# Performance work log

Hardware: AMD Instinct MI355X
Metric: run time of the kernel (lower is better)

The kernel has to match this reference:

```python
import jax, jax.numpy as jnp
import numpy as np

FACTORS = (32, 32, 32)  # prod = 32768 feature dim
BATCH = 2048


def setup_inputs() -> dict:
    key = jax.random.key(0)
    k0, k1, k2, k3 = jax.random.split(key, 4)
    N = int(np.prod(FACTORS))
    x = jax.random.normal(k0, (BATCH, N), dtype=jnp.float32)
    # scale weights ~1/sqrt(f) so outputs stay O(1) through 3 contractions
    s = 1.0 / np.sqrt(FACTORS[0])
    W1 = jax.random.normal(k1, (FACTORS[0], FACTORS[0]), dtype=jnp.float32) * s
    W2 = jax.random.normal(k2, (FACTORS[1], FACTORS[1]), dtype=jnp.float32) * s
    W3 = jax.random.normal(k3, (FACTORS[2], FACTORS[2]), dtype=jnp.float32) * s
    return {"x": x, "W1": W1, "W2": W2, "W3": W3}


def reference(x, W1, W2, W3):
    # Factorized (Kronecker) linear: y = x with each factor axis contracted
    # against its factor matrix (x.view(-1, f) @ W_f per factor, axes cycled).
    B = x.shape[0]
    f1, f2, f3 = FACTORS
    x = x.reshape(B, f1, f2, f3)
    x = jnp.einsum('bpqr,pi->biqr', x, W1)  # contract factor-1 axis
    x = jnp.einsum('biqr,qj->bijr', x, W2)  # contract factor-2 axis
    x = jnp.einsum('bijr,rk->bijk', x, W3)  # contract factor-3 axis
    return x.reshape(B, f1 * f2 * f3)
```

## Files before the change

### kernel.cpp

```cpp
#include <hip/hip_runtime.h>
#include <hip/hip_bf16.h>


typedef __attribute__((ext_vector_type(8))) short bf16x8;
typedef __attribute__((ext_vector_type(4))) float f32x4;

#define NROW 32768
#define NBLK 512

#define BAR() do {                                          \
    asm volatile("s_waitcnt lgkmcnt(0)" ::: "memory");      \
    __builtin_amdgcn_s_barrier();                           \
    __builtin_amdgcn_sched_barrier(0);                      \
} while (0)

__device__ __forceinline__ unsigned pk2(float a, float b) {
    union { __hip_bfloat162 h; unsigned u; } v;
    v.h = __float22bfloat162_rn(make_float2(a, b));
    return v.u;
}
__device__ __forceinline__ unsigned short b16(float a) {
    union { __hip_bfloat16 h; unsigned short u; } v;
    v.h = __float2bfloat16(a);
    return v.u;
}
__device__ __forceinline__ bf16x8 packfrag(float4 f0, float4 f1) {
    union { unsigned u[4]; bf16x8 b; } r;
    r.u[0] = pk2(f0.x, f0.y); r.u[1] = pk2(f0.z, f0.w);
    r.u[2] = pk2(f1.x, f1.y); r.u[3] = pk2(f1.z, f1.w);
    return r.b;
}

__device__ __forceinline__ int swz(int row, int col) {
    int s = ((row ^ (row >> 2) ^ (row >> 4)) & 3) << 3;
    return row * 32 + (col ^ s);
}

__device__ __forceinline__ bf16x8 ldsfrag(const unsigned short* buf, int row, int g) {
    int s = (row ^ (row >> 2) ^ (row >> 4)) & 3;
    union { uint4 u; bf16x8 b; } cv;
    cv.u = *(const uint4*)(buf + row * 32 + 8 * (g ^ s));
    return cv.b;
}

__global__ __launch_bounds__(1024, 8) void kron3_mfma(
    const float* __restrict__ x,  const float* __restrict__ W1,
    const float* __restrict__ W2, const float* __restrict__ W3,
    float* __restrict__ out, int iters)
{
    __shared__ unsigned short buf[NROW];
    __shared__ unsigned short wlds[3 * 1024];
    const int t = threadIdx.x;
    const int w = t >> 6, c = t & 15, g = (t >> 4) & 3;
    const f32x4 vzero = {0.f, 0.f, 0.f, 0.f};

    {
        const int n = t >> 5, k = t & 31;
        wlds[0 * 1024 + swz(n, k)] = b16(W1[k * 32 + n]);
        wlds[1 * 1024 + swz(n, k)] = b16(W2[k * 32 + n]);
        wlds[2 * 1024 + swz(n, k)] = b16(W3[k * 32 + n]);
    }
    BAR();

#pragma unroll 1
    for (int it = 0; it < iters; ++it) {
        int tv = t;
        asm volatile("" : "+v"(tv));
        const int cv = tv & 15, gv = (tv >> 4) & 3;
        const size_t row = (size_t)blockIdx.x + (size_t)NBLK * it;

        bf16x8 fa[4];
        {
            const float* xr = x + row * NROW;
#pragma unroll
            for (int mt = 0; mt < 4; ++mt) {
                const float* s = xr + (64 * w + 16 * mt + c) * 32 + 8 * g;
                float4 f0 = ((const float4*)s)[0];
                float4 f1 = ((const float4*)s)[1];
                fa[mt] = packfrag(f0, f1);
            }
        }

        {
            bf16x8 wA0 = ldsfrag(wlds + 2048, cv, gv);
            bf16x8 wA1 = ldsfrag(wlds + 2048, 16 + cv, gv);
#pragma unroll
            for (int nt = 0; nt < 2; ++nt) {
                const int kp = 16 * nt + c;
                const bf16x8 wA = nt ? wA1 : wA0;
#pragma unroll
                for (int mt = 0; mt < 4; ++mt) {
                    f32x4 a = __builtin_amdgcn_mfma_f32_16x16x32_bf16(fa[mt], wA, vzero, 0, 0, 0);
                    const int p  = 2 * w + (mt >> 1);
                    const int q0 = 16 * (mt & 1) + 4 * g;
                    *(uint2*)(buf + swz(p * 32 + kp, q0)) =
                        make_uint2(pk2(a[0], a[1]), pk2(a[2], a[3]));
                }
            }
        }

        bf16x8 fb[4];
#pragma unroll
        for (int mt = 0; mt < 4; ++mt)
            fb[mt] = ldsfrag(buf, 64 * w + 16 * mt + c, g);
        BAR();

        {
            bf16x8 wB0 = ldsfrag(wlds + 1024, cv, gv);
            bf16x8 wB1 = ldsfrag(wlds + 1024, 16 + cv, gv);
#pragma unroll
            for (int jt = 0; jt < 2; ++jt) {
                const bf16x8 wB = jt ? wB1 : wB0;
#pragma unroll
                for (int mt = 0; mt < 4; ++mt) {
                    f32x4 a = __builtin_amdgcn_mfma_f32_16x16x32_bf16(wB, fb[mt], vzero, 0, 0, 0);
                    const int k = 16 * (mt & 1) + c;
                    const int p = 2 * w + (mt >> 1);
#pragma unroll
                    for (int rg = 0; rg < 4; ++rg)
                        buf[swz((16 * jt + 4 * g + rg) * 32 + k, p)] = b16(a[rg]);
                }
            }
        }
        BAR();

        bf16x8 fc[4];
#pragma unroll
        for (int mt = 0; mt < 4; ++mt)
            fc[mt] = ldsfrag(buf, 64 * w + 16 * mt + c, g);
        BAR();

        {
            bf16x8 wC0 = ldsfrag(wlds, cv, gv);
            bf16x8 wC1 = ldsfrag(wlds, 16 + cv, gv);
            float* orow = out + row * NROW;
#pragma unroll
            for (int nt = 0; nt < 2; ++nt) {
                const int i = 16 * nt + c;
                const bf16x8 wC = nt ? wC1 : wC0;
#pragma unroll
                for (int mt = 0; mt < 4; ++mt) {
                    f32x4 a = __builtin_amdgcn_mfma_f32_16x16x32_bf16(fc[mt], wC, vzero, 0, 0, 0);
                    const int j  = 2 * w + (mt >> 1);
                    const int k0 = 16 * (mt & 1) + 4 * g;
                    *(float4*)(orow + i * 1024 + j * 32 + k0) =
                        make_float4(a[0], a[1], a[2], a[3]);
                }
            }
        }
    }
}

extern "C" void kernel_launch(void* const* d_in, const int* in_sizes, int n_in,
                              void* d_out, int out_size, void* d_ws, size_t ws_size,
                              hipStream_t stream) {
    const float* x  = (const float*)d_in[0];
    const float* W1 = (const float*)d_in[1];
    const float* W2 = (const float*)d_in[2];
    const float* W3 = (const float*)d_in[3];
    float* outp = (float*)d_out;

    const int batch = in_sizes[0] / NROW;
    const int iters = batch / NBLK;
    kron3_mfma<<<dim3(NBLK), dim3(1024), 0, stream>>>(x, W1, W2, W3, outp, iters);
}
```

Baseline: 149.6 us.

## Software-pipeline next-row x loads across stages and restructure LDS layout

The kernel now prefetches the next batch row's x fragments in two halves, overlapping them with the MFMA stages of the current row, and converts them to bf16 later. The intermediate LDS layout is changed so that stage 2 writes vectorized uint2 stores instead of scalar bf16 stores. Output stores use nontemporal hints. The intent is to hide global load latency and cut LDS store count, at the cost of extra registers for the prefetched float4 values and an added barrier.

```diff
diff --git a/kernel.cpp b/kernel.cpp
--- a/kernel.cpp
+++ b/kernel.cpp
@@ -43,7 +43,7 @@
     return cv.b;
 }
 
-__global__ __launch_bounds__(1024, 8) void kron3_mfma(
+__global__ __launch_bounds__(1024, 8) void kron3_pipe(
     const float* __restrict__ x,  const float* __restrict__ W1,
     const float* __restrict__ W2, const float* __restrict__ W3,
     float* __restrict__ out, int iters)
@@ -60,6 +60,20 @@
         wlds[1 * 1024 + swz(n, k)] = b16(W2[k * 32 + n]);
         wlds[2 * 1024 + swz(n, k)] = b16(W3[k * 32 + n]);
     }
+
+    float4 fr[8];
+    bf16x8 fa[4];
+    {
+        const float* xr = x + (size_t)blockIdx.x * NROW;
+#pragma unroll
+        for (int mt = 0; mt < 4; ++mt) {
+            const float* s = xr + (64 * w + 16 * mt + c) * 32 + 8 * g;
+            fr[2 * mt]     = ((const float4*)s)[0];
+            fr[2 * mt + 1] = ((const float4*)s)[1];
+        }
+#pragma unroll
+        for (int mt = 0; mt < 4; ++mt) fa[mt] = packfrag(fr[2 * mt], fr[2 * mt + 1]);
+    }
     BAR();
 
 #pragma unroll 1
@@ -68,18 +82,8 @@
         asm volatile("" : "+v"(tv));
         const int cv = tv & 15, gv = (tv >> 4) & 3;
         const size_t row = (size_t)blockIdx.x + (size_t)NBLK * it;
-
-        bf16x8 fa[4];
-        {
-            const float* xr = x + row * NROW;
-#pragma unroll
-            for (int mt = 0; mt < 4; ++mt) {
-                const float* s = xr + (64 * w + 16 * mt + c) * 32 + 8 * g;
-                float4 f0 = ((const float4*)s)[0];
-                float4 f1 = ((const float4*)s)[1];
-                fa[mt] = packfrag(f0, f1);
-            }
-        }
+        const bool pre = (it + 1 < iters);
+        const float* xnext = x + (row + NBLK) * NROW;
 
         {
             bf16x8 wA0 = ldsfrag(wlds + 2048, cv, gv);
@@ -93,11 +97,20 @@
                     f32x4 a = __builtin_amdgcn_mfma_f32_16x16x32_bf16(fa[mt], wA, vzero, 0, 0, 0);
                     const int p  = 2 * w + (mt >> 1);
                     const int q0 = 16 * (mt & 1) + 4 * g;
-                    *(uint2*)(buf + swz(p * 32 + kp, q0)) =
+                    *(uint2*)(buf + swz(kp * 32 + p, q0)) =
                         make_uint2(pk2(a[0], a[1]), pk2(a[2], a[3]));
                 }
             }
         }
+        if (pre) {
+#pragma unroll
+            for (int mt = 0; mt < 2; ++mt) {
+                const float* s = xnext + (64 * w + 16 * mt + c) * 32 + 8 * g;
+                fr[2 * mt]     = ((const float4*)s)[0];
+                fr[2 * mt + 1] = ((const float4*)s)[1];
+            }
+        }
+        BAR();
 
         bf16x8 fb[4];
 #pragma unroll
@@ -109,17 +122,27 @@
             bf16x8 wB0 = ldsfrag(wlds + 1024, cv, gv);
             bf16x8 wB1 = ldsfrag(wlds + 1024, 16 + cv, gv);
 #pragma unroll
-            for (int jt = 0; jt < 2; ++jt) {
-                const bf16x8 wB = jt ? wB1 : wB0;
+            for (int nt = 0; nt < 2; ++nt) {
+                const int j = 16 * nt + c;
+                const bf16x8 wB = nt ? wB1 : wB0;
 #pragma unroll
                 for (int mt = 0; mt < 4; ++mt) {
-                    f32x4 a = __builtin_amdgcn_mfma_f32_16x16x32_bf16(wB, fb[mt], vzero, 0, 0, 0);
-                    const int k = 16 * (mt & 1) + c;
-                    const int p = 2 * w + (mt >> 1);
+                    f32x4 a = __builtin_amdgcn_mfma_f32_16x16x32_bf16(fb[mt], wB, vzero, 0, 0, 0);
+                    const int kq = 2 * w + (mt >> 1);
+                    const int p0 = 16 * (mt & 1) + 4 * g;
+                    *(uint2*)(buf + swz(j * 32 + kq, p0)) =
+                        make_uint2(pk2(a[0], a[1]), pk2(a[2], a[3]));
+                }
+            }
+        }
+        if (pre) {
+            fa[0] = packfrag(fr[0], fr[1]);
+            fa[1] = packfrag(fr[2], fr[3]);
 #pragma unroll
-                    for (int rg = 0; rg < 4; ++rg)
-                        buf[swz((16 * jt + 4 * g + rg) * 32 + k, p)] = b16(a[rg]);
-                }
+            for (int mt = 2; mt < 4; ++mt) {
+                const float* s = xnext + (64 * w + 16 * mt + c) * 32 + 8 * g;
+                fr[2 * mt]     = ((const float4*)s)[0];
+                fr[2 * mt + 1] = ((const float4*)s)[1];
             }
         }
         BAR();
@@ -143,10 +166,14 @@
                     f32x4 a = __builtin_amdgcn_mfma_f32_16x16x32_bf16(fc[mt], wC, vzero, 0, 0, 0);
                     const int j  = 2 * w + (mt >> 1);
                     const int k0 = 16 * (mt & 1) + 4 * g;
-                    *(float4*)(orow + i * 1024 + j * 32 + k0) =
-                        make_float4(a[0], a[1], a[2], a[3]);
+                    __builtin_nontemporal_store(a,
+                        (f32x4*)(orow + i * 1024 + j * 32 + k0));
                 }
             }
+        }
+        if (pre) {
+            fa[2] = packfrag(fr[4], fr[5]);
+            fa[3] = packfrag(fr[6], fr[7]);
         }
     }
 }
@@ -162,5 +189,5 @@
 
     const int batch = in_sizes[0] / NROW;
     const int iters = batch / NBLK;
-    kron3_mfma<<<dim3(NBLK), dim3(1024), 0, stream>>>(x, W1, W2, W3, outp, iters);
+    kron3_pipe<<<dim3(NBLK), dim3(1024), 0, stream>>>(x, W1, W2, W3, outp, iters);
 }
```

After: 255.5 us. +70.8%, slower.
